# Optimization experiments

Hardware: AMD Instinct MI355X
Metric: run time of the kernel (lower is better)

Reference implementation:

```python
import jax, jax.numpy as jnp
import numpy as np


def setup_inputs() -> dict:
    key = jax.random.key(0)
    kq, kk, kv = jax.random.split(key, 3)
    B, QH, KH, S, D = 2, 32, 8, 2048, 128
    Q = jax.random.normal(kq, (B, QH, S, D), dtype=jnp.float32)
    K = jax.random.normal(kk, (B, KH, S, D), dtype=jnp.float32)
    V = jax.random.normal(kv, (B, KH, S, D), dtype=jnp.float32)
    return {"Q": Q, "K": K, "V": V}


def reference(Q, K, V):
    B, QH, S, D = Q.shape
    KH = K.shape[1]
    G = QH // KH  # group size: query heads per KV head
    scale = jnp.sqrt(jnp.asarray(D, dtype=Q.dtype))
    # Group query heads: [B, KH, G, S, D]
    Qg = Q.reshape(B, KH, G, S, D)
    # scores: [B, KH, G, S, S]
    scores = jnp.einsum('bkgsd,bktd->bkgst', Qg, K) / scale
    probs = jax.nn.softmax(scores, axis=-1)
    out = jnp.einsum('bkgst,bktd->bkgsd', probs, V)
    return out.reshape(B, QH, S, D)
```

## Files before the change

kernel.cpp:

```cpp
#include <hip/hip_runtime.h>

typedef unsigned short u16;
typedef unsigned int u32;
typedef u16 u16x4 __attribute__((ext_vector_type(4)));
typedef u16 u16x8 __attribute__((ext_vector_type(8)));
typedef u32 u32x4 __attribute__((ext_vector_type(4)));
typedef __bf16 bf16x8 __attribute__((ext_vector_type(8)));
typedef float f32x4 __attribute__((ext_vector_type(4)));

#define NB   2
#define NQH  32
#define NKH  8
#define SEQ  2048
#define DIM  128
#define BKV  64
#define QT   64
#define NTILE   (SEQ / BKV)
#define TILEU16 (BKV * DIM)
#define VOFFU16 (16 * NTILE * TILEU16)

__device__ __forceinline__ u16 f2bf(float f) {
  u32 u = __builtin_bit_cast(u32, f);
  u += 0x7FFFu + ((u >> 16) & 1u);
  return (u16)(u >> 16);
}
__device__ __forceinline__ u32 cvtpk(float lo, float hi) {
  u32 r;
  asm("v_cvt_pk_bf16_f32 %0, %1, %2" : "=v"(r) : "v"(lo), "v"(hi));
  return r;
}
__device__ __forceinline__ f32x4 mfma16(u16x8 a, u16x8 b, f32x4 c) {
  return __builtin_amdgcn_mfma_f32_16x16x32_bf16(
      __builtin_bit_cast(bf16x8, a), __builtin_bit_cast(bf16x8, b), c, 0, 0, 0);
}
__device__ __forceinline__ const u16* lds_at(const u16* base, int row, int col, int rowU16) {
  return base + row * rowU16 + (col ^ ((row & 7) << 3));
}
__device__ __forceinline__ void gl_lds16(const u16* g, u16* l) {
  __builtin_amdgcn_global_load_lds(
      (const __attribute__((address_space(1))) u32*)(const void*)g,
      (__attribute__((address_space(3))) u32*)(void*)l, 16, 0, 0);
}

__global__ __launch_bounds__(256) void prep(const float* __restrict__ Kg,
                                            const float* __restrict__ Vg,
                                            u16* __restrict__ ws) {
  const int bid = blockIdx.x;
  const int tid = threadIdx.x;
  const int tile = bid & 511;
  const size_t sbase = (size_t)(tile >> 5) * SEQ * DIM + (size_t)(tile & 31) * BKV * DIM;
  if (bid < 512) {
    const float* src = Kg + sbase;
    u16* img = ws + (size_t)tile * TILEU16;
    #pragma unroll
    for (int u = 0; u < 8; ++u) {
      int c = tid + 256 * u;
      int j = c >> 5;
      int dm = (c & 31) * 4;
      float4 v = *(const float4*)(src + j * DIM + dm);
      u16x4 w = { f2bf(v.x), f2bf(v.y), f2bf(v.z), f2bf(v.w) };
      *(u16x4*)(img + j * 128 + (dm ^ ((j & 7) << 3))) = w;
    }
  } else {
    const float* src = Vg + sbase;
    u16* img = ws + VOFFU16 + (size_t)tile * TILEU16;
    #pragma unroll
    for (int u = 0; u < 4; ++u) {
      int c = tid + 256 * u;
      int d = c >> 3;
      int cc = c & 7;
      u16x8 w;
      #pragma unroll
      for (int i = 0; i < 8; ++i) {
        int s = 8 * cc + i;
        int key = 32 * (s >> 5) + 4 * ((s >> 3) & 3) + 16 * (i >> 2) + (i & 3);
        w[i] = f2bf(src[key * DIM + d]);
      }
      *(u16x8*)(img + d * 64 + ((8 * cc) ^ ((d & 7) << 3))) = w;
    }
  }
}

__global__ __launch_bounds__(256) void gqa_fwd(const float* __restrict__ Qg,
                                               const u16* __restrict__ ws,
                                               float* __restrict__ Og) {
  __shared__ __align__(16) u16 ldsK[TILEU16];
  __shared__ __align__(16) u16 ldsVT[TILEU16];

  const int tid  = threadIdx.x;
  const int lane = tid & 63;
  const int wave = tid >> 6;
  const int lr   = lane & 15;
  const int lg   = lane >> 4;

  const int qtile = blockIdx.x;
  const int bqh   = blockIdx.y;
  const int b     = bqh / NQH;
  const int qh    = bqh % NQH;
  const int kh    = qh / (NQH / NKH);

  const size_t qbase = (size_t)bqh * SEQ * DIM;
  const u16* imgK = ws + (size_t)((b * NKH + kh) * NTILE) * TILEU16;
  const u16* imgV = imgK + VOFFU16;

  const int qrow0 = qtile * QT + wave * 16;
  const float scale = 0.08838834764831845f;

  u16x8 qf[4];
  #pragma unroll
  for (int s = 0; s < 4; ++s) {
    const float* qp = Qg + qbase + (size_t)(qrow0 + lr) * DIM + 32 * s + 8 * lg;
    float4 a = *(const float4*)qp;
    float4 c = *(const float4*)(qp + 4);
    qf[s] = __builtin_bit_cast(u16x8, u32x4{
        cvtpk(a.x * scale, a.y * scale), cvtpk(a.z * scale, a.w * scale),
        cvtpk(c.x * scale, c.y * scale), cvtpk(c.z * scale, c.w * scale) });
  }

  const f32x4 zero4 = {0.f, 0.f, 0.f, 0.f};
  f32x4 oacc[8];
  #pragma unroll
  for (int dt = 0; dt < 8; ++dt) oacc[dt] = zero4;
  float mrow = -1e30f, lrow = 0.0f;

  for (int kt = 0; kt < NTILE; ++kt) {
    __syncthreads();
    #pragma unroll
    for (int u = 0; u < 4; ++u) {
      const int q = u * 4 + wave;
      gl_lds16(imgK + (size_t)kt * TILEU16 + q * 512 + lane * 8, &ldsK[q * 512]);
      gl_lds16(imgV + (size_t)kt * TILEU16 + q * 512 + lane * 8, &ldsVT[q * 512]);
    }
    asm volatile("s_waitcnt vmcnt(0)" ::: "memory");
    __syncthreads();

    f32x4 sacc[4];
    #pragma unroll
    for (int jt = 0; jt < 4; ++jt) sacc[jt] = zero4;
    #pragma unroll
    for (int jt = 0; jt < 4; ++jt) {
      #pragma unroll
      for (int s = 0; s < 4; ++s) {
        u16x8 kf = *(const u16x8*)lds_at(ldsK, jt * 16 + lr, 32 * s + 8 * lg, 128);
        sacc[jt] = mfma16(kf, qf[s], sacc[jt]);
      }
    }

    float tmax = sacc[0][0];
    #pragma unroll
    for (int jt = 0; jt < 4; ++jt)
      #pragma unroll
      for (int e = 0; e < 4; ++e) tmax = fmaxf(tmax, sacc[jt][e]);
    tmax = fmaxf(tmax, __shfl_xor(tmax, 16, 64));
    tmax = fmaxf(tmax, __shfl_xor(tmax, 32, 64));

    if (!__all(tmax - mrow <= 8.0f)) {
      float mn = fmaxf(mrow, tmax);
      float corr = __expf(mrow - mn);
      mrow = mn;
      lrow *= corr;
      float corr_o[4];
      #pragma unroll
      for (int e = 0; e < 4; ++e) corr_o[e] = __shfl(corr, 4 * lg + e, 64);
      #pragma unroll
      for (int dt = 0; dt < 8; ++dt)
        #pragma unroll
        for (int e = 0; e < 4; ++e) oacc[dt][e] *= corr_o[e];
    }

    u32 pk[8];
    float rsum = 0.f;
    #pragma unroll
    for (int jt = 0; jt < 4; ++jt) {
      float p0 = __expf(sacc[jt][0] - mrow);
      float p1 = __expf(sacc[jt][1] - mrow);
      float p2 = __expf(sacc[jt][2] - mrow);
      float p3 = __expf(sacc[jt][3] - mrow);
      rsum += (p0 + p1) + (p2 + p3);
      pk[2 * jt]     = cvtpk(p0, p1);
      pk[2 * jt + 1] = cvtpk(p2, p3);
    }
    rsum += __shfl_xor(rsum, 16, 64);
    rsum += __shfl_xor(rsum, 32, 64);
    lrow += rsum;

    u16x8 af[2];
    af[0] = __builtin_bit_cast(u16x8, u32x4{pk[0], pk[1], pk[2], pk[3]});
    af[1] = __builtin_bit_cast(u16x8, u32x4{pk[4], pk[5], pk[6], pk[7]});
    #pragma unroll
    for (int dt = 0; dt < 8; ++dt) {
      #pragma unroll
      for (int ks = 0; ks < 2; ++ks) {
        u16x8 vf = *(const u16x8*)lds_at(ldsVT, dt * 16 + lr, 32 * ks + 8 * lg, 64);
        oacc[dt] = mfma16(af[ks], vf, oacc[dt]);
      }
    }
  }

  float linv = 1.0f / lrow;
  float linv_o[4];
  #pragma unroll
  for (int e = 0; e < 4; ++e) linv_o[e] = __shfl(linv, 4 * lg + e, 64);
  #pragma unroll
  for (int e = 0; e < 4; ++e) {
    int row = qrow0 + 4 * lg + e;
    float* op = Og + qbase + (size_t)row * DIM;
    #pragma unroll
    for (int dt = 0; dt < 8; ++dt) op[dt * 16 + lr] = oacc[dt][e] * linv_o[e];
  }
}

extern "C" void kernel_launch(void* const* d_in, const int* in_sizes, int n_in,
                              void* d_out, int out_size, void* d_ws, size_t ws_size,
                              hipStream_t stream) {
  const float* Q = (const float*)d_in[0];
  const float* K = (const float*)d_in[1];
  const float* V = (const float*)d_in[2];
  float* O = (float*)d_out;
  u16* ws = (u16*)d_ws;
  prep<<<dim3(1024), 256, 0, stream>>>(K, V, ws);
  dim3 grid(SEQ / QT, NB * NQH);
  gqa_fwd<<<grid, 256, 0, stream>>>(Q, ws, O);
}
```

Before: 207.2 us.

## Switch to 32x32 MFMA with double-buffered K/V tiles and larger Q tile

```diff
diff --git a/kernel.cpp b/kernel.cpp
--- a/kernel.cpp
+++ b/kernel.cpp
@@ -6,7 +6,7 @@
 typedef u16 u16x8 __attribute__((ext_vector_type(8)));
 typedef u32 u32x4 __attribute__((ext_vector_type(4)));
 typedef __bf16 bf16x8 __attribute__((ext_vector_type(8)));
-typedef float f32x4 __attribute__((ext_vector_type(4)));
+typedef float f32x16 __attribute__((ext_vector_type(16)));
 
 #define NB   2
 #define NQH  32
@@ -14,7 +14,7 @@
 #define SEQ  2048
 #define DIM  128
 #define BKV  64
-#define QT   64
+#define QT   128
 #define NTILE   (SEQ / BKV)
 #define TILEU16 (BKV * DIM)
 #define VOFFU16 (16 * NTILE * TILEU16)
@@ -29,12 +29,9 @@
   asm("v_cvt_pk_bf16_f32 %0, %1, %2" : "=v"(r) : "v"(lo), "v"(hi));
   return r;
 }
-__device__ __forceinline__ f32x4 mfma16(u16x8 a, u16x8 b, f32x4 c) {
-  return __builtin_amdgcn_mfma_f32_16x16x32_bf16(
+__device__ __forceinline__ f32x16 mfma32(u16x8 a, u16x8 b, f32x16 c) {
+  return __builtin_amdgcn_mfma_f32_32x32x16_bf16(
       __builtin_bit_cast(bf16x8, a), __builtin_bit_cast(bf16x8, b), c, 0, 0, 0);
-}
-__device__ __forceinline__ const u16* lds_at(const u16* base, int row, int col, int rowU16) {
-  return base + row * rowU16 + (col ^ ((row & 7) << 3));
 }
 __device__ __forceinline__ void gl_lds16(const u16* g, u16* l) {
   __builtin_amdgcn_global_load_lds(
@@ -68,15 +65,15 @@
     for (int u = 0; u < 4; ++u) {
       int c = tid + 256 * u;
       int d = c >> 3;
-      int cc = c & 7;
+      int pg = c & 7;
       u16x8 w;
       #pragma unroll
       for (int i = 0; i < 8; ++i) {
-        int s = 8 * cc + i;
-        int key = 32 * (s >> 5) + 4 * ((s >> 3) & 3) + 16 * (i >> 2) + (i & 3);
+        int p = 8 * pg + i;
+        int key = (p & ~12) | ((p & 8) >> 1) | ((p & 4) << 1);
         w[i] = f2bf(src[key * DIM + d]);
       }
-      *(u16x8*)(img + d * 64 + ((8 * cc) ^ ((d & 7) << 3))) = w;
+      *(u16x8*)(img + d * 64 + ((8 * pg) ^ ((d & 7) << 3))) = w;
     }
   }
 }
@@ -84,129 +81,145 @@
 __global__ __launch_bounds__(256) void gqa_fwd(const float* __restrict__ Qg,
                                                const u16* __restrict__ ws,
                                                float* __restrict__ Og) {
-  __shared__ __align__(16) u16 ldsK[TILEU16];
-  __shared__ __align__(16) u16 ldsVT[TILEU16];
+  __shared__ __align__(16) u16 sK[2][TILEU16];
+  __shared__ __align__(16) u16 sV[2][TILEU16];
 
   const int tid  = threadIdx.x;
   const int lane = tid & 63;
   const int wave = tid >> 6;
-  const int lr   = lane & 15;
-  const int lg   = lane >> 4;
-
-  const int qtile = blockIdx.x;
-  const int bqh   = blockIdx.y;
-  const int b     = bqh / NQH;
-  const int qh    = bqh % NQH;
-  const int kh    = qh / (NQH / NKH);
+  const int l31  = lane & 31;
+  const int h    = lane >> 5;
+
+  const int id = blockIdx.x;
+  const int wg = (id & 7) * 128 + (id >> 3);
+  const int qtile = wg & 15;
+  const int bqh   = wg >> 4;
+  const int b     = bqh >> 5;
+  const int qh    = bqh & 31;
+  const int kh    = qh >> 2;
 
   const size_t qbase = (size_t)bqh * SEQ * DIM;
   const u16* imgK = ws + (size_t)((b * NKH + kh) * NTILE) * TILEU16;
   const u16* imgV = imgK + VOFFU16;
-
-  const int qrow0 = qtile * QT + wave * 16;
-  const float scale = 0.08838834764831845f;
-
-  u16x8 qf[4];
+  const int qrow_w = qtile * QT + wave * 32;
+
+  const float s2 = 0.08838834764831845f * 1.4426950408889634f;
+
+  u16x8 qf[8];
   #pragma unroll
-  for (int s = 0; s < 4; ++s) {
-    const float* qp = Qg + qbase + (size_t)(qrow0 + lr) * DIM + 32 * s + 8 * lg;
+  for (int s8 = 0; s8 < 8; ++s8) {
+    const float* qp = Qg + qbase + (size_t)(qrow_w + l31) * DIM + 16 * s8 + 8 * h;
     float4 a = *(const float4*)qp;
     float4 c = *(const float4*)(qp + 4);
-    qf[s] = __builtin_bit_cast(u16x8, u32x4{
-        cvtpk(a.x * scale, a.y * scale), cvtpk(a.z * scale, a.w * scale),
-        cvtpk(c.x * scale, c.y * scale), cvtpk(c.z * scale, c.w * scale) });
-  }
-
-  const f32x4 zero4 = {0.f, 0.f, 0.f, 0.f};
-  f32x4 oacc[8];
+    qf[s8] = __builtin_bit_cast(u16x8, u32x4{
+        cvtpk(a.x * s2, a.y * s2), cvtpk(a.z * s2, a.w * s2),
+        cvtpk(c.x * s2, c.y * s2), cvtpk(c.z * s2, c.w * s2) });
+  }
+
+  f32x16 oacc[4];
   #pragma unroll
-  for (int dt = 0; dt < 8; ++dt) oacc[dt] = zero4;
-  float mrow = -1e30f, lrow = 0.0f;
-
-  for (int kt = 0; kt < NTILE; ++kt) {
-    __syncthreads();
+  for (int dt = 0; dt < 4; ++dt)
+    #pragma unroll
+    for (int r = 0; r < 16; ++r) oacc[dt][r] = 0.f;
+  float mrow = -3.0e38f, lrow = 0.f;
+
+  auto issue = [&](int nk, int pb) {
+    const u16* gK = imgK + (size_t)nk * TILEU16;
+    const u16* gV = imgV + (size_t)nk * TILEU16;
     #pragma unroll
     for (int u = 0; u < 4; ++u) {
       const int q = u * 4 + wave;
-      gl_lds16(imgK + (size_t)kt * TILEU16 + q * 512 + lane * 8, &ldsK[q * 512]);
-      gl_lds16(imgV + (size_t)kt * TILEU16 + q * 512 + lane * 8, &ldsVT[q * 512]);
-    }
-    asm volatile("s_waitcnt vmcnt(0)" ::: "memory");
-    __syncthreads();
-
-    f32x4 sacc[4];
-    #pragma unroll
-    for (int jt = 0; jt < 4; ++jt) sacc[jt] = zero4;
-    #pragma unroll
-    for (int jt = 0; jt < 4; ++jt) {
-      #pragma unroll
-      for (int s = 0; s < 4; ++s) {
-        u16x8 kf = *(const u16x8*)lds_at(ldsK, jt * 16 + lr, 32 * s + 8 * lg, 128);
-        sacc[jt] = mfma16(kf, qf[s], sacc[jt]);
-      }
-    }
-
-    float tmax = sacc[0][0];
-    #pragma unroll
-    for (int jt = 0; jt < 4; ++jt)
-      #pragma unroll
-      for (int e = 0; e < 4; ++e) tmax = fmaxf(tmax, sacc[jt][e]);
-    tmax = fmaxf(tmax, __shfl_xor(tmax, 16, 64));
+      gl_lds16(gK + q * 512 + lane * 8, &sK[pb][q * 512]);
+      gl_lds16(gV + q * 512 + lane * 8, &sV[pb][q * 512]);
+    }
+  };
+
+  auto tile_body = [&](int KT, int PB) {
+    issue((KT + 1) & 31, PB ^ 1);
+    asm volatile("s_waitcnt vmcnt(8)" ::: "memory");
+    __builtin_amdgcn_s_barrier();
+
+    f32x16 sac0, sac1;
+    #pragma unroll
+    for (int r = 0; r < 16; ++r) { sac0[r] = 0.f; sac1[r] = 0.f; }
+    const int swz = (l31 & 7) << 3;
+    __builtin_amdgcn_s_setprio(1);
+    #pragma unroll
+    for (int s8 = 0; s8 < 8; ++s8) {
+      u16x8 kf0 = *(const u16x8*)&sK[PB][l31 * 128 + ((16 * s8 + 8 * h) ^ swz)];
+      u16x8 kf1 = *(const u16x8*)&sK[PB][(32 + l31) * 128 + ((16 * s8 + 8 * h) ^ swz)];
+      sac0 = mfma32(kf0, qf[s8], sac0);
+      sac1 = mfma32(kf1, qf[s8], sac1);
+    }
+    __builtin_amdgcn_s_setprio(0);
+
+    float tmax = -3.0e38f;
+    #pragma unroll
+    for (int r = 0; r < 16; ++r) tmax = fmaxf(tmax, fmaxf(sac0[r], sac1[r]));
     tmax = fmaxf(tmax, __shfl_xor(tmax, 32, 64));
 
-    if (!__all(tmax - mrow <= 8.0f)) {
+    if (!__all(tmax - mrow <= 11.0f)) {
       float mn = fmaxf(mrow, tmax);
-      float corr = __expf(mrow - mn);
+      float corr = exp2f(mrow - mn);
       mrow = mn;
       lrow *= corr;
-      float corr_o[4];
       #pragma unroll
-      for (int e = 0; e < 4; ++e) corr_o[e] = __shfl(corr, 4 * lg + e, 64);
-      #pragma unroll
-      for (int dt = 0; dt < 8; ++dt)
-        #pragma unroll
-        for (int e = 0; e < 4; ++e) oacc[dt][e] *= corr_o[e];
-    }
-
-    u32 pk[8];
+      for (int r = 0; r < 16; ++r) {
+        float co = __shfl(corr, (r & 3) + 8 * (r >> 2) + 4 * h, 64);
+        oacc[0][r] *= co; oacc[1][r] *= co; oacc[2][r] *= co; oacc[3][r] *= co;
+      }
+    }
+
     float rsum = 0.f;
     #pragma unroll
-    for (int jt = 0; jt < 4; ++jt) {
-      float p0 = __expf(sacc[jt][0] - mrow);
-      float p1 = __expf(sacc[jt][1] - mrow);
-      float p2 = __expf(sacc[jt][2] - mrow);
-      float p3 = __expf(sacc[jt][3] - mrow);
-      rsum += (p0 + p1) + (p2 + p3);
-      pk[2 * jt]     = cvtpk(p0, p1);
-      pk[2 * jt + 1] = cvtpk(p2, p3);
-    }
-    rsum += __shfl_xor(rsum, 16, 64);
+    for (int r = 0; r < 16; ++r) {
+      sac0[r] = exp2f(sac0[r] - mrow);
+      sac1[r] = exp2f(sac1[r] - mrow);
+      rsum += sac0[r] + sac1[r];
+    }
     rsum += __shfl_xor(rsum, 32, 64);
     lrow += rsum;
 
-    u16x8 af[2];
-    af[0] = __builtin_bit_cast(u16x8, u32x4{pk[0], pk[1], pk[2], pk[3]});
-    af[1] = __builtin_bit_cast(u16x8, u32x4{pk[4], pk[5], pk[6], pk[7]});
-    #pragma unroll
-    for (int dt = 0; dt < 8; ++dt) {
+    u16x8 af[4];
+    af[0] = __builtin_bit_cast(u16x8, u32x4{cvtpk(sac0[0], sac0[1]),  cvtpk(sac0[2], sac0[3]),
+                                            cvtpk(sac0[4], sac0[5]),  cvtpk(sac0[6], sac0[7])});
+    af[1] = __builtin_bit_cast(u16x8, u32x4{cvtpk(sac0[8], sac0[9]),  cvtpk(sac0[10], sac0[11]),
+                                            cvtpk(sac0[12], sac0[13]), cvtpk(sac0[14], sac0[15])});
+    af[2] = __builtin_bit_cast(u16x8, u32x4{cvtpk(sac1[0], sac1[1]),  cvtpk(sac1[2], sac1[3]),
+                                            cvtpk(sac1[4], sac1[5]),  cvtpk(sac1[6], sac1[7])});
+    af[3] = __builtin_bit_cast(u16x8, u32x4{cvtpk(sac1[8], sac1[9]),  cvtpk(sac1[10], sac1[11]),
+                                            cvtpk(sac1[12], sac1[13]), cvtpk(sac1[14], sac1[15])});
+
+    __builtin_amdgcn_s_setprio(1);
+    #pragma unroll
+    for (int dt = 0; dt < 4; ++dt) {
       #pragma unroll
-      for (int ks = 0; ks < 2; ++ks) {
-        u16x8 vf = *(const u16x8*)lds_at(ldsVT, dt * 16 + lr, 32 * ks + 8 * lg, 64);
-        oacc[dt] = mfma16(af[ks], vf, oacc[dt]);
+      for (int c = 0; c < 4; ++c) {
+        u16x8 vf = *(const u16x8*)&sV[PB][(32 * dt + l31) * 64 + ((16 * c + 8 * h) ^ swz)];
+        oacc[dt] = mfma32(af[c], vf, oacc[dt]);
       }
     }
-  }
+    __builtin_amdgcn_s_setprio(0);
+    __builtin_amdgcn_s_barrier();
+  };
+
+  issue(0, 0);
+  for (int kt2 = 0; kt2 < 16; ++kt2) {
+    tile_body(2 * kt2, 0);
+    tile_body(2 * kt2 + 1, 1);
+  }
+  asm volatile("s_waitcnt vmcnt(0)" ::: "memory");
 
   float linv = 1.0f / lrow;
-  float linv_o[4];
   #pragma unroll
-  for (int e = 0; e < 4; ++e) linv_o[e] = __shfl(linv, 4 * lg + e, 64);
-  #pragma unroll
-  for (int e = 0; e < 4; ++e) {
-    int row = qrow0 + 4 * lg + e;
-    float* op = Og + qbase + (size_t)row * DIM;
-    #pragma unroll
-    for (int dt = 0; dt < 8; ++dt) op[dt * 16 + lr] = oacc[dt][e] * linv_o[e];
+  for (int r = 0; r < 16; ++r) {
+    const int ql = (r & 3) + 8 * (r >> 2) + 4 * h;
+    float li = __shfl(linv, ql, 64);
+    float* op = Og + qbase + (size_t)(qrow_w + ql) * DIM + l31;
+    op[0]  = oacc[0][r] * li;
+    op[32] = oacc[1][r] * li;
+    op[64] = oacc[2][r] * li;
+    op[96] = oacc[3][r] * li;
   }
 }
 
@@ -219,6 +232,5 @@
   float* O = (float*)d_out;
   u16* ws = (u16*)d_ws;
   prep<<<dim3(1024), 256, 0, stream>>>(K, V, ws);
-  dim3 grid(SEQ / QT, NB * NQH);
-  gqa_fwd<<<grid, 256, 0, stream>>>(Q, ws, O);
-}
+  gqa_fwd<<<dim3((SEQ / QT) * NB * NQH), 256, 0, stream>>>(Q, ws, O);
+}
```

Measured after the change: 284.0 us. +37.1%, slower.
